# Performance work log

Measured on AMD Instinct MI355X. Metric: run time of the kernel, lower is better.

## Reference

```python
import jax, jax.numpy as jnp
import numpy as np

D = 64      # hidden_dim
H = 4       # num_attention_heads
DH = D // H # head_dim
B = 64      # graphs per batch
SCALE = np.float32(np.sqrt(DH))


def _sage(x, edge, wl, bl, wr):
    # SAGEConv: lin_l(mean_j x_j) + lin_r(x_i); mean over incoming edges (dst = edge[1])
    src, dst = edge[0], edge[1]
    n = x.shape[0]
    agg = jax.ops.segment_sum(x[src], dst, num_segments=n)
    cnt = jax.ops.segment_sum(jnp.ones((edge.shape[1],), x.dtype), dst, num_segments=n)
    mean = agg / jnp.maximum(cnt, 1.0)[:, None]
    return mean @ wl + bl + x @ wr


def _cross_attn(xq, xk, w, b):
    # w: [3, D, D] stacked (Q, K, V) projections; b: [3, D]
    Q = (xq @ w[0] + b[0]).reshape(-1, H, DH)  # [Nq, H, DH]
    K = (xk @ w[1] + b[1]).reshape(-1, H, DH)  # [Nk, H, DH]
    V = (xk @ w[2] + b[2]).reshape(-1, H, DH)
    scores = jnp.einsum('qhd,khd->hqk', Q, K) / SCALE  # [H, Nq, Nk]
    wgt = jax.nn.softmax(scores, axis=-1)
    out = jnp.einsum('hqk,khd->qhd', wgt, V)
    return out.reshape(xq.shape[0], D)


def _segment_mean(x, seg, num):
    s = jax.ops.segment_sum(x, seg, num_segments=num)
    c = jax.ops.segment_sum(jnp.ones((x.shape[0],), x.dtype), seg, num_segments=num)
    return s / jnp.maximum(c, 1.0)[:, None]


def setup_inputs() -> dict:
    key = jax.random.key(0)
    ks = jax.random.split(key, 32)
    N_MOL, N_PROT, E_MOL, E_PROT = 2048, 8192, 32768, 131072
    MOL_IN, PROT_IN = 32, 64

    def lin(k, i, o, s=None):
        s = 1.0 / np.sqrt(i) if s is None else s
        return (jax.random.normal(k, (i, o), jnp.float32) * s)

    inp = {
        'x_mol': jax.random.normal(ks[0], (N_MOL, MOL_IN), jnp.float32),
        'x_prot': jax.random.normal(ks[1], (N_PROT, PROT_IN), jnp.float32),
        'm1_wl': lin(ks[2], MOL_IN, D), 'm1_bl': jnp.zeros((D,), jnp.float32), 'm1_wr': lin(ks[3], MOL_IN, D),
        'm2_wl': lin(ks[4], D, D), 'm2_bl': jnp.zeros((D,), jnp.float32), 'm2_wr': lin(ks[5], D, D),
        'p1_wl': lin(ks[6], PROT_IN, D), 'p1_bl': jnp.zeros((D,), jnp.float32), 'p1_wr': lin(ks[7], PROT_IN, D),
        'p2_wl': lin(ks[8], D, D), 'p2_bl': jnp.zeros((D,), jnp.float32), 'p2_wr': lin(ks[9], D, D),
        'amp_w': jax.random.normal(ks[10], (3, D, D), jnp.float32) / np.sqrt(D),
        'amp_b': jnp.zeros((3, D), jnp.float32),
        'apm_w': jax.random.normal(ks[11], (3, D, D), jnp.float32) / np.sqrt(D),
        'apm_b': jnp.zeros((3, D), jnp.float32),
        'fc1_w': lin(ks[12], 2 * D, D), 'fc1_b': jnp.zeros((D,), jnp.float32),
        'fc2_w': lin(ks[13], D, 1), 'fc2_b': jnp.zeros((1,), jnp.float32),
        'edge_mol': jax.random.randint(ks[14], (2, E_MOL), 0, N_MOL, jnp.int32),
        'edge_prot': jax.random.randint(ks[15], (2, E_PROT), 0, N_PROT, jnp.int32),
        'batch_mol': jnp.sort(jax.random.randint(ks[16], (N_MOL,), 0, B, jnp.int32)),
        'batch_prot': jnp.sort(jax.random.randint(ks[17], (N_PROT,), 0, B, jnp.int32)),
    }
    return inp


def reference(x_mol, x_prot,
              m1_wl, m1_bl, m1_wr, m2_wl, m2_bl, m2_wr,
              p1_wl, p1_bl, p1_wr, p2_wl, p2_bl, p2_wr,
              amp_w, amp_b, apm_w, apm_b,
              fc1_w, fc1_b, fc2_w, fc2_b,
              edge_mol, edge_prot, batch_mol, batch_prot):
    # two SAGE conv blocks per graph, ReLU after each (HeteroConv with one edge type)
    h_mol = jax.nn.relu(_sage(x_mol, edge_mol, m1_wl, m1_bl, m1_wr))
    h_mol = jax.nn.relu(_sage(h_mol, edge_mol, m2_wl, m2_bl, m2_wr))
    h_prot = jax.nn.relu(_sage(x_prot, edge_prot, p1_wl, p1_bl, p1_wr))
    h_prot = jax.nn.relu(_sage(h_prot, edge_prot, p2_wl, p2_bl, p2_wr))
    # cross attention (mol queries prot, prot queries mol) + residual
    h_mol_c = h_mol + _cross_attn(h_mol, h_prot, amp_w, amp_b)
    h_prot_c = h_prot + _cross_attn(h_prot, h_mol, apm_w, apm_b)
    # global mean pool per graph
    z_mol = _segment_mean(h_mol_c, batch_mol, B)    # [B, D]
    z_prot = _segment_mean(h_prot_c, batch_prot, B)  # [B, D]
    z = jnp.concatenate([z_mol, z_prot], axis=1)     # [B, 2D]
    x = jax.nn.relu(z @ fc1_w + fc1_b)
    out = jax.nn.sigmoid(x @ fc2_w + fc2_b)
    return out.squeeze(-1)  # [B]
```

## Files before the change

### kernel.cpp

```cpp
#include <hip/hip_runtime.h>
#include <math.h>

#define D 64
#define NB 64

typedef __attribute__((ext_vector_type(8))) short bf16x8;
typedef __attribute__((ext_vector_type(4))) float f32x4;
typedef __attribute__((ext_vector_type(16))) float f32x16;

#define M3(a, b, c) fmaxf(fmaxf((a), (b)), (c))

__device__ __forceinline__ unsigned short f2bf(float f) {
    unsigned u = __float_as_uint(f);
    u += 0x7FFF + ((u >> 16) & 1);
    return (unsigned short)(u >> 16);
}
__device__ __forceinline__ unsigned pk_bf16(float lo, float hi) {
    unsigned r;
    asm("v_cvt_pk_bf16_f32 %0, %1, %2" : "=v"(r) : "v"(lo), "v"(hi));
    return r;
}
__device__ __forceinline__ float fexp2(float x) {
    float r;
    asm("v_exp_f32 %0, %1" : "=v"(r) : "v"(x));
    return r;
}

__global__ void k_prep2(const int* __restrict__ em, int Em,
                        const int* __restrict__ ep, int Ep,
                        int* __restrict__ degm, int* __restrict__ degp,
                        const int* __restrict__ bm, int Nm, int* __restrict__ bsM,
                        const int* __restrict__ bp, int Np, int* __restrict__ bsP) {
    int i = blockIdx.x * blockDim.x + threadIdx.x;
    if (i < Em) atomicAdd(&degm[em[Em + i]], 1);
    int j = i - Em;
    if (j >= 0 && j < Ep) atomicAdd(&degp[ep[Ep + j]], 1);
    if (i < Nm) {
        int cur = bm[i];
        int prev = (i == 0) ? -1 : bm[i - 1];
        for (int b = prev + 1; b <= cur; ++b) bsM[b] = i;
        if (i == Nm - 1)
            for (int b = cur + 1; b <= NB; ++b) bsM[b] = Nm;
    }
    int j2 = i - Nm;
    if (j2 >= 0 && j2 < Np) {
        int cur = bp[j2];
        int prev = (j2 == 0) ? -1 : bp[j2 - 1];
        for (int b = prev + 1; b <= cur; ++b) bsP[b] = j2;
        if (j2 == Np - 1)
            for (int b = cur + 1; b <= NB; ++b) bsP[b] = Np;
    }
}

__global__ __launch_bounds__(256) void k_scan2(
        const int* __restrict__ degm, int Nm, int* __restrict__ rpm, int* __restrict__ curm,
        const int* __restrict__ degp, int Np, int* __restrict__ rpp, int* __restrict__ curp) {
    __shared__ int sdeg[8192];
    __shared__ int chunk[256];
    const int* deg = blockIdx.x ? degp : degm;
    int N = blockIdx.x ? Np : Nm;
    int* rowptr = blockIdx.x ? rpp : rpm;
    int* cursor = blockIdx.x ? curp : curm;
    int t = threadIdx.x;
    for (int i = t; i < N; i += 256) sdeg[i] = deg[i];
    __syncthreads();
    int C = (N + 255) / 256;
    int start = t * C;
    int sum = 0;
    for (int i = 0; i < C; ++i)
        if (start + i < N) sum += sdeg[start + i];
    chunk[t] = sum;
    __syncthreads();
    for (int ofs = 1; ofs < 256; ofs <<= 1) {
        int v = (t >= ofs) ? chunk[t - ofs] : 0;
        __syncthreads();
        chunk[t] += v;
        __syncthreads();
    }
    int base = (t == 0) ? 0 : chunk[t - 1];
    for (int i = 0; i < C && start + i < N; ++i) {
        rowptr[start + i] = base;
        cursor[start + i] = base;
        base += sdeg[start + i];
    }
    if (t == 255) rowptr[N] = base;
}

__global__ void k_scatter2(const int* __restrict__ em, int Em, int* __restrict__ curm,
                           int* __restrict__ csrm,
                           const int* __restrict__ ep, int Ep, int* __restrict__ curp,
                           int* __restrict__ csrp) {
    int i = blockIdx.x * blockDim.x + threadIdx.x;
    if (i < Em) {
        int s = em[i], d = em[Em + i];
        csrm[atomicAdd(&curm[d], 1)] = s;
    }
    int j = i - Em;
    if (j >= 0 && j < Ep) {
        int s = ep[j], d = ep[Ep + j];
        csrp[atomicAdd(&curp[d], 1)] = s;
    }
}

template<int FIN>
__device__ __forceinline__ void gsage_body(
        const float* __restrict__ x, const int* __restrict__ rowptr,
        const int* __restrict__ csr, int N,
        const float* __restrict__ wl, const float* __restrict__ bl,
        const float* __restrict__ wr, float* __restrict__ out,
        int blk, float* __restrict__ swl, float* __restrict__ swr,
        float* __restrict__ sagg, float* __restrict__ sx) {
    for (int i = threadIdx.x; i < FIN * D; i += 256) { swl[i] = wl[i]; swr[i] = wr[i]; }
    int w = threadIdx.x >> 6;
    int lane = threadIdx.x & 63;
    int r = blk * 4 + w;
    if (r < N) {
        int e0 = rowptr[r], e1 = rowptr[r + 1];
        float inv = 1.0f / fmaxf((float)(e1 - e0), 1.0f);
        if (FIN == 64) {
            float a0 = 0.f, a1 = 0.f, a2 = 0.f, a3 = 0.f;
            int e = e0;
            for (; e + 3 < e1; e += 4) {
                a0 += x[(size_t)csr[e] * FIN + lane];
                a1 += x[(size_t)csr[e + 1] * FIN + lane];
                a2 += x[(size_t)csr[e + 2] * FIN + lane];
                a3 += x[(size_t)csr[e + 3] * FIN + lane];
            }
            for (; e < e1; ++e) a0 += x[(size_t)csr[e] * FIN + lane];
            sagg[w * 64 + lane] = ((a0 + a1) + (a2 + a3)) * inv;
            sx[w * 64 + lane] = x[(size_t)r * FIN + lane];
        } else {
            int f = lane & 31, half = lane >> 5;
            float a = 0.f;
            for (int e = e0 + half; e < e1; e += 2)
                a += x[(size_t)csr[e] * FIN + f];
            a += __shfl_xor(a, 32);
            if (half == 0) {
                sagg[w * 64 + f] = a * inv;
                sx[w * 64 + f] = x[(size_t)r * FIN + f];
            }
        }
    }
    __syncthreads();
    if (r >= N) return;
    int c = lane;
    float acc = bl[c];
    #pragma unroll 8
    for (int k = 0; k < FIN; ++k) {
        acc += sagg[w * 64 + k] * swl[k * D + c];
        acc += sx[w * 64 + k] * swr[k * D + c];
    }
    out[(size_t)r * D + c] = fmaxf(acc, 0.0f);
}

template<int FA, int FB>
__global__ __launch_bounds__(256) void k_gsage2(
        const float* __restrict__ xA, const int* __restrict__ rpA,
        const int* __restrict__ csrA, int NA,
        const float* __restrict__ wlA, const float* __restrict__ blA,
        const float* __restrict__ wrA, float* __restrict__ outA,
        const float* __restrict__ xB, const int* __restrict__ rpB,
        const int* __restrict__ csrB, int NB_,
        const float* __restrict__ wlB, const float* __restrict__ blB,
        const float* __restrict__ wrB, float* __restrict__ outB) {
    __shared__ float swl[64 * 64];
    __shared__ float swr[64 * 64];
    __shared__ float sagg[4 * 64];
    __shared__ float sx[4 * 64];
    int bA = NA / 4;
    if ((int)blockIdx.x < bA)
        gsage_body<FA>(xA, rpA, csrA, NA, wlA, blA, wrA, outA, blockIdx.x, swl, swr, sagg, sx);
    else
        gsage_body<FB>(xB, rpB, csrB, NB_, wlB, blB, wrB, outB, blockIdx.x - bA, swl, swr, sagg, sx);
}

__global__ __launch_bounds__(256) void k_qkv2(
        const float* __restrict__ xA, int NA, const float* __restrict__ xB, int NB_,
        const float* __restrict__ amp_w, const float* __restrict__ amp_b,
        const float* __restrict__ apm_w, const float* __restrict__ apm_b, float qs,
        unsigned short* __restrict__ QA, unsigned short* __restrict__ KA, unsigned short* __restrict__ VA,
        unsigned short* __restrict__ QB, unsigned short* __restrict__ KB, unsigned short* __restrict__ VB) {
    __shared__ float sq[D * D], sk[D * D], sv[D * D], sx[16 * D];
    int bA = NA / 16;
    const float *x, *wq, *bq, *wk, *bk, *wv, *bv;
    unsigned short *oq, *ok, *ov;
    int blk;
    if ((int)blockIdx.x < bA) {
        x = xA; blk = blockIdx.x;
        wq = amp_w;        bq = amp_b;
        wk = apm_w + 4096; bk = apm_b + 64;
        wv = apm_w + 8192; bv = apm_b + 128;
        oq = QA; ok = KA; ov = VA;
    } else {
        x = xB; blk = blockIdx.x - bA;
        wq = apm_w;        bq = apm_b;
        wk = amp_w + 4096; bk = amp_b + 64;
        wv = amp_w + 8192; bv = amp_b + 128;
        oq = QB; ok = KB; ov = VB;
    }
    for (int i = threadIdx.x; i < D * D; i += 256) { sq[i] = wq[i]; sk[i] = wk[i]; sv[i] = wv[i]; }
    int rbase = blk * 16;
    for (int i = threadIdx.x; i < 16 * D; i += 256) sx[i] = x[(size_t)rbase * D + i];
    __syncthreads();
    int c = threadIdx.x & 63;
    int r0 = (threadIdx.x >> 6) * 4;
    for (int rr = 0; rr < 4; ++rr) {
        int r = r0 + rr;
        float aq = bq[c], ak = bk[c], av = bv[c];
        #pragma unroll 8
        for (int k = 0; k < D; ++k) {
            float xv = sx[r * D + k];
            aq += xv * sq[k * D + c];
            ak += xv * sk[k * D + c];
            av += xv * sv[k * D + c];
        }
        size_t o = (size_t)(rbase + r) * D + c;
        oq[o] = f2bf(aq * qs);
        ok[o] = f2bf(ak);
        ov[o] = f2bf(av);
    }
}

__global__ void k_transp2(const unsigned short* __restrict__ inM, unsigned short* __restrict__ outM, int Nm,
                          const unsigned short* __restrict__ inP, unsigned short* __restrict__ outP, int Np) {
    __shared__ unsigned short tile[64][72];
    int bm = Nm >> 6;
    const unsigned short* in; unsigned short* out; int N;
    int blk = blockIdx.x;
    if (blk < bm) { in = inM; out = outM; N = Nm; }
    else { blk -= bm; in = inP; out = outP; N = Np; }
    int t = threadIdx.x;
    int rbase = blk * 64;
    {
        int r = t >> 2, c0 = (t & 3) * 16;
        const uint4* src = (const uint4*)(in + (size_t)(rbase + r) * 64 + c0);
        uint4 a = src[0], b = src[1];
        *(uint4*)(&tile[r][c0]) = a;
        *(uint4*)(&tile[r][c0 + 8]) = b;
    }
    __syncthreads();
    {
        int c = t >> 2, r0 = (t & 3) * 16;
        union { uint2 v2[4]; unsigned short s[16]; } u;
        #pragma unroll
        for (int i = 0; i < 16; ++i) u.s[i] = tile[r0 + i][c];
        int key0 = rbase + r0;
        int kc = key0 & ~31;
        int b16 = key0 & 16;
        unsigned short* op = out + (size_t)c * N;
        const int gmap[4] = {0, 8, 4, 12};
        #pragma unroll
        for (int b = 0; b < 4; ++b)
            *(uint2*)(op + kc + b16 + gmap[b]) = u.v2[b];
    }
    if (t < 8) {
        uint4 ones;
        ones.x = ones.y = ones.z = ones.w = 0x3F803F80u;
        *(uint4*)(out + (size_t)64 * N + rbase + t * 8) = ones;
    }
}

#define MAXTREE(cm, s0, s1)                                                   \
    {                                                                         \
        float c0 = M3(s0[0], s0[1], s0[2]);                                   \
        float c1 = M3(s0[3], s0[4], s0[5]);                                   \
        float c2 = M3(s0[6], s0[7], s0[8]);                                   \
        float c3 = M3(s0[9], s0[10], s0[11]);                                 \
        float c4 = M3(s0[12], s0[13], s0[14]);                                \
        float c5 = M3(s0[15], s1[0], s1[1]);                                  \
        float c6 = M3(s1[2], s1[3], s1[4]);                                   \
        float c7 = M3(s1[5], s1[6], s1[7]);                                   \
        float c8 = M3(s1[8], s1[9], s1[10]);                                  \
        float c9 = M3(s1[11], s1[12], s1[13]);                                \
        float ca = fmaxf(s1[14], s1[15]);                                     \
        float d0 = M3(c0, c1, c2);                                            \
        float d1 = M3(c3, c4, c5);                                            \
        float d2 = M3(c6, c7, c8);                                            \
        float d3 = M3(c9, ca, d0);                                            \
        cm = M3(d1, d2, d3);                                                  \
    }

#define PVPACK(S, KB)                                                         \
    {                                                                         \
        union { unsigned u[4]; bf16x8 v; } f1, f2;                            \
        f1.u[0] = pk_bf16((S)[0], (S)[1]);   f1.u[1] = pk_bf16((S)[2], (S)[3]);  \
        f1.u[2] = pk_bf16((S)[4], (S)[5]);   f1.u[3] = pk_bf16((S)[6], (S)[7]);  \
        f2.u[0] = pk_bf16((S)[8], (S)[9]);   f2.u[1] = pk_bf16((S)[10], (S)[11]);\
        f2.u[2] = pk_bf16((S)[12], (S)[13]); f2.u[3] = pk_bf16((S)[14], (S)[15]);\
        bf16x8 vb0 = *(const bf16x8*)(vbase + (KB) + half * 8);               \
        bf16x8 vb1 = *(const bf16x8*)(vbase + (KB) + 16 + half * 8);          \
        __builtin_amdgcn_s_setprio(1);                                        \
        o = __builtin_amdgcn_mfma_f32_32x32x16_bf16(f1.v, vb0, o, 0, 0, 0);   \
        o = __builtin_amdgcn_mfma_f32_32x32x16_bf16(f2.v, vb1, o, 0, 0, 0);   \
        __builtin_amdgcn_s_setprio(0);                                        \
    }

__global__ __launch_bounds__(512) void k_attn6(
        const unsigned short* __restrict__ QmB, const unsigned short* __restrict__ KpB,
        const unsigned short* __restrict__ VpT, int Nm, int Np, int lsm,
        float* __restrict__ poM, float* __restrict__ pmM, float* __restrict__ plM,
        const unsigned short* __restrict__ QpB, const unsigned short* __restrict__ KmB,
        const unsigned short* __restrict__ VmT, int lsp,
        float* __restrict__ poP, float* __restrict__ pmP, float* __restrict__ plP) {
    const unsigned short *Q, *K, *Vt;
    int Nq, Nk, ls;
    float *po, *pm, *pl;
    if (blockIdx.y == 0) { Q = QmB; K = KpB; Vt = VpT; Nq = Nm; Nk = Np; ls = lsm; po = poM; pm = pmM; pl = plM; }
    else                 { Q = QpB; K = KmB; Vt = VmT; Nq = Np; Nk = Nm; ls = lsp; po = poP; pm = pmP; pl = plP; }
    int npair = Nq >> 6;
    if ((int)blockIdx.x >= (npair << ls)) return;
    const int qpair = blockIdx.x >> ls;
    const int split = blockIdx.x & ((1 << ls) - 1);
    const int kchunk = Nk >> ls;
    const int w = threadIdx.x >> 6;
    const int h = w & 3;
    const int qt = qpair * 2 + (w >> 2);
    const int lane = threadIdx.x & 63;
    const int cq = lane & 31;
    const int half = lane >> 5;
    const int h16 = h * 16;

    bf16x8 qb = *(const bf16x8*)(Q + ((size_t)(qt * 32 + cq) * D + h16 + half * 8));
    int drow = (cq < 16) ? (h16 + cq) : (cq == 16 ? 64 : h16 + 15);
    const unsigned short* vbase = Vt + (size_t)drow * Nk;

    f32x16 o, mC;
    #pragma unroll
    for (int i = 0; i < 16; ++i) { o[i] = 0.f; mC[i] = 0.f; }
    float m;

    const int kstart = split * kchunk;
    {
        const int kb = kstart;
        bf16x8 ka0 = *(const bf16x8*)(K + ((size_t)(kb + cq) * D + h16 + half * 8));
        bf16x8 ka1 = *(const bf16x8*)(K + ((size_t)(kb + 32 + cq) * D + h16 + half * 8));
        f32x16 s0 = __builtin_amdgcn_mfma_f32_32x32x16_bf16(ka0, qb, mC, 0, 0, 0);
        f32x16 s1 = __builtin_amdgcn_mfma_f32_32x32x16_bf16(ka1, qb, mC, 0, 0, 0);
        float cm;
        MAXTREE(cm, s0, s1);
        #pragma unroll
        for (int off = 1; off < 64; off <<= 1) cm = fmaxf(cm, __shfl_xor(cm, off));
        m = cm;
        #pragma unroll
        for (int i = 0; i < 16; ++i) {
            s0[i] = fexp2(s0[i] - m);
            s1[i] = fexp2(s1[i] - m);
            mC[i] = -m;
        }
        PVPACK(s0, kb)
        PVPACK(s1, kb + 32)
    }
    for (int kb = kstart + 64; kb < kstart + kchunk; kb += 64) {
        bf16x8 ka0 = *(const bf16x8*)(K + ((size_t)(kb + cq) * D + h16 + half * 8));
        bf16x8 ka1 = *(const bf16x8*)(K + ((size_t)(kb + 32 + cq) * D + h16 + half * 8));
        f32x16 s0 = __builtin_amdgcn_mfma_f32_32x32x16_bf16(ka0, qb, mC, 0, 0, 0);
        f32x16 s1 = __builtin_amdgcn_mfma_f32_32x32x16_bf16(ka1, qb, mC, 0, 0, 0);
        float cm;
        MAXTREE(cm, s0, s1);
        if (__any(cm > 8.f)) {
            float cw = cm;
            #pragma unroll
            for (int off = 1; off < 64; off <<= 1) cw = fmaxf(cw, __shfl_xor(cw, off));
            float nm = fmaxf(m + cw, m);
            float sc = fexp2(m - nm);
            #pragma unroll
            for (int i = 0; i < 16; ++i) o[i] *= sc;
            float dl = nm - m;
            #pragma unroll
            for (int i = 0; i < 16; ++i) { s0[i] -= dl; s1[i] -= dl; mC[i] = -nm; }
            m = nm;
        }
        #pragma unroll
        for (int i = 0; i < 16; ++i) { s0[i] = fexp2(s0[i]); s1[i] = fexp2(s1[i]); }
        PVPACK(s0, kb)
        PVPACK(s1, kb + 32)
    }

    size_t pbase = (size_t)split * Nq + qt * 32;
    if (half == 0)
        pm[(pbase + cq) * 4 + h] = m;
    if (cq == 16) {
        #pragma unroll
        for (int r = 0; r < 16; ++r) {
            int qr = (r & 3) + 8 * (r >> 2) + 4 * half;
            pl[(pbase + qr) * 4 + h] = o[r];
        }
    }
    if (cq < 16) {
        #pragma unroll
        for (int r = 0; r < 16; ++r) {
            int qr = (r & 3) + 8 * (r >> 2) + 4 * half;
            po[(pbase + qr) * 64 + h16 + cq] = o[r];
        }
    }
}

template<int NS>
__device__ __forceinline__ void comb_body(
        const float* __restrict__ po, const float* __restrict__ pm,
        const float* __restrict__ pl, int Nq,
        const float* __restrict__ resid, float* __restrict__ outc, int i) {
    int q = i >> 4;
    int part = i & 15;
    int d0 = part * 4;
    int h = part >> 2;
    float pmv[NS], plv[NS];
    #pragma unroll
    for (int s = 0; s < NS; ++s) pmv[s] = pm[((size_t)s * Nq + q) * 4 + h];
    #pragma unroll
    for (int s = 0; s < NS; ++s) plv[s] = pl[((size_t)s * Nq + q) * 4 + h];
    float M = pmv[0];
    #pragma unroll
    for (int s = 1; s < NS; ++s) M = fmaxf(M, pmv[s]);
    float4 O = {0.f, 0.f, 0.f, 0.f};
    float L = 0.f;
    #pragma unroll
    for (int s = 0; s < NS; ++s) {
        float wgt = fexp2(pmv[s] - M);
        float4 pv = *(const float4*)(po + ((size_t)s * Nq + q) * 64 + d0);
        O.x += pv.x * wgt; O.y += pv.y * wgt; O.z += pv.z * wgt; O.w += pv.w * wgt;
        L += plv[s] * wgt;
    }
    float invL = 1.0f / L;
    float4 rv = *(const float4*)(resid + (size_t)q * 64 + d0);
    float4 res;
    res.x = rv.x + O.x * invL;
    res.y = rv.y + O.y * invL;
    res.z = rv.z + O.z * invL;
    res.w = rv.w + O.w * invL;
    *(float4*)(outc + (size_t)q * 64 + d0) = res;
}

template<int NSM, int NSP>
__global__ void k_comb2t(
        const float* __restrict__ poM, const float* __restrict__ pmM, const float* __restrict__ plM,
        int Nm, const float* __restrict__ residM, float* __restrict__ outM,
        const float* __restrict__ poP, const float* __restrict__ pmP, const float* __restrict__ plP,
        int Np, const float* __restrict__ residP, float* __restrict__ outP) {
    int idx = blockIdx.x * blockDim.x + threadIdx.x;
    int mtot = Nm * 16;
    if (idx < mtot)
        comb_body<NSM>(poM, pmM, plM, Nm, residM, outM, idx);
    else if (idx - mtot < Np * 16)
        comb_body<NSP>(poP, pmP, plP, Np, residP, outP, idx - mtot);
}

__global__ void k_comb2(
        const float* __restrict__ poM, const float* __restrict__ pmM, const float* __restrict__ plM,
        int nsM, int Nm, const float* __restrict__ residM, float* __restrict__ outM,
        const float* __restrict__ poP, const float* __restrict__ pmP, const float* __restrict__ plP,
        int nsP, int Np, const float* __restrict__ residP, float* __restrict__ outP) {
    int idx = blockIdx.x * blockDim.x + threadIdx.x;
    const float *po, *pm, *pl, *resid;
    float* outc;
    int ns, Nq, i;
    int mtot = Nm * 64;
    if (idx < mtot) {
        po = poM; pm = pmM; pl = plM; ns = nsM; Nq = Nm; resid = residM; outc = outM; i = idx;
    } else {
        i = idx - mtot;
        if (i >= Np * 64) return;
        po = poP; pm = pmP; pl = plP; ns = nsP; Nq = Np; resid = residP; outc = outP;
    }
    int q = i >> 6, d = i & 63, h = d >> 4;
    float M = -1e30f;
    for (int s = 0; s < ns; ++s)
        M = fmaxf(M, pm[((size_t)s * Nq + q) * 4 + h]);
    float O = 0.f, L = 0.f;
    for (int s = 0; s < ns; ++s) {
        float wgt = fexp2(pm[((size_t)s * Nq + q) * 4 + h] - M);
        O += po[((size_t)s * Nq + q) * 64 + d] * wgt;
        L += pl[((size_t)s * Nq + q) * 4 + h] * wgt;
    }
    outc[i] = resid[i] + O / L;
}

__global__ __launch_bounds__(256) void k_pool2(
        const float* __restrict__ hM, const int* __restrict__ bsM,
        const float* __restrict__ hP, const int* __restrict__ bsP,
        float* __restrict__ zsum, float* __restrict__ zcnt) {
    __shared__ float red[4][64];
    int b = blockIdx.x & 63;
    int isP = blockIdx.x >> 6;
    const float* h = isP ? hP : hM;
    const int* bs = isP ? bsP : bsM;
    int colOff = isP ? 64 : 0;
    int n0 = bs[b], n1 = bs[b + 1];
    int w = threadIdx.x >> 6, c = threadIdx.x & 63;
    float acc = 0.f;
    for (int n = n0 + w; n < n1; n += 4)
        acc += h[(size_t)n * 64 + c];
    red[w][c] = acc;
    __syncthreads();
    if (w == 0) {
        float s = (red[0][c] + red[1][c]) + (red[2][c] + red[3][c]);
        zsum[b * 128 + colOff + c] = s;
        if (c == 0) zcnt[b * 2 + isP] = (float)(n1 - n0);
    }
}

__global__ __launch_bounds__(256) void k_head2(
        const float* __restrict__ zsum, const float* __restrict__ zcnt,
        const float* __restrict__ fc1w, const float* __restrict__ fc1b,
        const float* __restrict__ fc2w, const float* __restrict__ fc2b,
        float* __restrict__ out) {
    int b = blockIdx.x * 4 + (threadIdx.x >> 6);
    int c = threadIdx.x & 63;
    float inv0 = 1.0f / fmaxf(zcnt[b * 2 + 0], 1.0f);
    float inv1 = 1.0f / fmaxf(zcnt[b * 2 + 1], 1.0f);
    float acc = fc1b[c];
    #pragma unroll 8
    for (int k = 0; k < 128; ++k) {
        float zv = zsum[b * 128 + k] * (k < 64 ? inv0 : inv1);
        acc += zv * fc1w[k * 64 + c];
    }
    float v = fmaxf(acc, 0.0f) * fc2w[c];
    #pragma unroll
    for (int off = 32; off > 0; off >>= 1) v += __shfl_xor(v, off);
    if (c == 0) out[b] = 1.0f / (1.0f + __expf(-(v + fc2b[0])));
}

extern "C" void kernel_launch(void* const* d_in, const int* in_sizes, int n_in,
                              void* d_out, int out_size, void* d_ws, size_t ws_size,
                              hipStream_t stream) {
    const float* x_mol  = (const float*)d_in[0];
    const float* x_prot = (const float*)d_in[1];
    const float* m1_wl = (const float*)d_in[2];
    const float* m1_bl = (const float*)d_in[3];
    const float* m1_wr = (const float*)d_in[4];
    const float* m2_wl = (const float*)d_in[5];
    const float* m2_bl = (const float*)d_in[6];
    const float* m2_wr = (const float*)d_in[7];
    const float* p1_wl = (const float*)d_in[8];
    const float* p1_bl = (const float*)d_in[9];
    const float* p1_wr = (const float*)d_in[10];
    const float* p2_wl = (const float*)d_in[11];
    const float* p2_bl = (const float*)d_in[12];
    const float* p2_wr = (const float*)d_in[13];
    const float* amp_w = (const float*)d_in[14];
    const float* amp_b = (const float*)d_in[15];
    const float* apm_w = (const float*)d_in[16];
    const float* apm_b = (const float*)d_in[17];
    const float* fc1_w = (const float*)d_in[18];
    const float* fc1_b = (const float*)d_in[19];
    const float* fc2_w = (const float*)d_in[20];
    const float* fc2_b = (const float*)d_in[21];
    const int* edge_mol  = (const int*)d_in[22];
    const int* edge_prot = (const int*)d_in[23];
    const int* batch_mol  = (const int*)d_in[24];
    const int* batch_prot = (const int*)d_in[25];
    float* out = (float*)d_out;

    const int N_MOL  = in_sizes[0] / 32;
    const int N_PROT = in_sizes[1] / 64;
    const int E_MOL  = in_sizes[22] / 2;
    const int E_PROT = in_sizes[23] / 2;

    char* base = (char*)d_ws;
    size_t off = 0;
    auto alloc = [&](size_t bytes) -> void* {
        void* p = base + off;
        off = (off + bytes + 255) & ~(size_t)255;
        return p;
    };
    float* h_mol1   = (float*)alloc((size_t)N_MOL * D * sizeof(float));
    float* h_mol2   = (float*)alloc((size_t)N_MOL * D * sizeof(float));
    float* h_prot1  = (float*)alloc((size_t)N_PROT * D * sizeof(float));
    float* h_prot2  = (float*)alloc((size_t)N_PROT * D * sizeof(float));
    float* h_mol_c  = (float*)alloc((size_t)N_MOL * D * sizeof(float));
    float* h_prot_c = (float*)alloc((size_t)N_PROT * D * sizeof(float));
    float* zsum     = (float*)alloc((NB * 128 + NB * 2) * sizeof(float));
    float* zcnt     = zsum + NB * 128;
    unsigned short* Qm_b = (unsigned short*)alloc((size_t)N_MOL * D * 2);
    unsigned short* Km_b = (unsigned short*)alloc((size_t)N_MOL * D * 2);
    unsigned short* Vm_b = (unsigned short*)alloc((size_t)N_MOL * D * 2);
    unsigned short* Vm_t = (unsigned short*)alloc((size_t)N_MOL * (D + 1) * 2);
    unsigned short* Qp_b = (unsigned short*)alloc((size_t)N_PROT * D * 2);
    unsigned short* Kp_b = (unsigned short*)alloc((size_t)N_PROT * D * 2);
    unsigned short* Vp_b = (unsigned short*)alloc((size_t)N_PROT * D * 2);
    unsigned short* Vp_t = (unsigned short*)alloc((size_t)N_PROT * (D + 1) * 2);
    int* deg      = (int*)alloc(((size_t)N_MOL + N_PROT) * sizeof(int));
    int* deg_m    = deg;
    int* deg_p    = deg + N_MOL;
    int* rp_m     = (int*)alloc(((size_t)N_MOL + 1) * sizeof(int));
    int* cur_m    = (int*)alloc((size_t)N_MOL * sizeof(int));
    int* csr_m    = (int*)alloc((size_t)E_MOL * sizeof(int));
    int* rp_p     = (int*)alloc(((size_t)N_PROT + 1) * sizeof(int));
    int* cur_p    = (int*)alloc((size_t)N_PROT * sizeof(int));
    int* csr_p    = (int*)alloc((size_t)E_PROT * sizeof(int));
    int* bsM      = (int*)alloc((NB + 1) * sizeof(int));
    int* bsP      = (int*)alloc((NB + 1) * sizeof(int));

    int nsm = 16; while (nsm > 1 && (N_PROT % (64 * nsm))) nsm >>= 1;
    int nsp = 4;  while (nsp > 1 && (N_MOL % (64 * nsp)))  nsp >>= 1;
    int lsm = 31 - __builtin_clz(nsm);
    int lsp = 31 - __builtin_clz(nsp);
    float* poM = (float*)alloc((size_t)nsm * N_MOL * 64 * sizeof(float));
    float* pmM = (float*)alloc((size_t)nsm * N_MOL * 4 * sizeof(float));
    float* plM = (float*)alloc((size_t)nsm * N_MOL * 4 * sizeof(float));
    float* poP = (float*)alloc((size_t)nsp * N_PROT * 64 * sizeof(float));
    float* pmP = (float*)alloc((size_t)nsp * N_PROT * 4 * sizeof(float));
    float* plP = (float*)alloc((size_t)nsp * N_PROT * 4 * sizeof(float));

    const int BLK = 256;
    dim3 blk(BLK);
    const float QS = 0.25f * 1.4426950408889634f;

    hipMemsetAsync(deg, 0, ((size_t)N_MOL + N_PROT) * sizeof(int), stream);
    int Etot = E_MOL + E_PROT;
    k_prep2<<<(Etot + BLK - 1) / BLK, blk, 0, stream>>>(
        edge_mol, E_MOL, edge_prot, E_PROT, deg_m, deg_p,
        batch_mol, N_MOL, bsM, batch_prot, N_PROT, bsP);
    k_scan2<<<2, blk, 0, stream>>>(deg_m, N_MOL, rp_m, cur_m, deg_p, N_PROT, rp_p, cur_p);
    k_scatter2<<<(Etot + BLK - 1) / BLK, blk, 0, stream>>>(edge_mol, E_MOL, cur_m, csr_m,
                                                           edge_prot, E_PROT, cur_p, csr_p);

    k_gsage2<32, 64><<<N_MOL / 4 + N_PROT / 4, blk, 0, stream>>>(
        x_mol,  rp_m, csr_m, N_MOL,  m1_wl, m1_bl, m1_wr, h_mol1,
        x_prot, rp_p, csr_p, N_PROT, p1_wl, p1_bl, p1_wr, h_prot1);
    k_gsage2<64, 64><<<N_MOL / 4 + N_PROT / 4, blk, 0, stream>>>(
        h_mol1,  rp_m, csr_m, N_MOL,  m2_wl, m2_bl, m2_wr, h_mol2,
        h_prot1, rp_p, csr_p, N_PROT, p2_wl, p2_bl, p2_wr, h_prot2);

    k_qkv2<<<N_MOL / 16 + N_PROT / 16, blk, 0, stream>>>(
        h_mol2, N_MOL, h_prot2, N_PROT, amp_w, amp_b, apm_w, apm_b, QS,
        Qm_b, Km_b, Vm_b, Qp_b, Kp_b, Vp_b);

    k_transp2<<<N_MOL / 64 + N_PROT / 64, blk, 0, stream>>>(Vm_b, Vm_t, N_MOL, Vp_b, Vp_t, N_PROT);

    int gxm = (N_MOL / 64) * nsm;
    int gxp = (N_PROT / 64) * nsp;
    int gx = gxm > gxp ? gxm : gxp;
    k_attn6<<<dim3(gx, 2), dim3(512), 0, stream>>>(
        Qm_b, Kp_b, Vp_t, N_MOL, N_PROT, lsm, poM, pmM, plM,
        Qp_b, Km_b, Vm_t, lsp, poP, pmP, plP);

    if (nsm == 16 && nsp == 4) {
        int tot = (N_MOL + N_PROT) * 16;
        k_comb2t<16, 4><<<(tot + BLK - 1) / BLK, blk, 0, stream>>>(
            poM, pmM, plM, N_MOL, h_mol2, h_mol_c,
            poP, pmP, plP, N_PROT, h_prot2, h_prot_c);
    } else {
        k_comb2<<<((N_MOL + N_PROT) * 64 + BLK - 1) / BLK, blk, 0, stream>>>(
            poM, pmM, plM, nsm, N_MOL, h_mol2, h_mol_c,
            poP, pmP, plP, nsp, N_PROT, h_prot2, h_prot_c);
    }

    k_pool2<<<128, blk, 0, stream>>>(h_mol_c, bsM, h_prot_c, bsP, zsum, zcnt);

    k_head2<<<16, blk, 0, stream>>>(zsum, zcnt, fc1_w, fc1_b, fc2_w, fc2_b, out);
}
```

Measured before the change: 171.9 us.

## Fuse V transpose into QKV, merge pool and head, batch SAGE rows

The V transpose now happens inside the QKV projection kernel: V is staged as bf16 in shared memory and written straight into the transposed, swizzled layout, including the ones row, so the separate transpose kernel and its intermediate buffer go away. Global pooling and the MLP head are merged into one kernel that runs one block per graph. The SAGE kernel now handles 16 rows per block instead of 4, so the weight load into shared memory is paid over more rows. This cuts two launches and some global traffic, but it lowers block counts and parallelism in the SAGE, QKV and pool kernels.

```diff
diff --git a/kernel.cpp b/kernel.cpp
--- a/kernel.cpp
+++ b/kernel.cpp
@@ -103,7 +103,7 @@
 }
 
 template<int FIN>
-__device__ __forceinline__ void gsage_body(
+__device__ __forceinline__ void gsage3_body(
         const float* __restrict__ x, const int* __restrict__ rowptr,
         const int* __restrict__ csr, int N,
         const float* __restrict__ wl, const float* __restrict__ bl,
@@ -111,10 +111,12 @@
         int blk, float* __restrict__ swl, float* __restrict__ swr,
         float* __restrict__ sagg, float* __restrict__ sx) {
     for (int i = threadIdx.x; i < FIN * D; i += 256) { swl[i] = wl[i]; swr[i] = wr[i]; }
+    __syncthreads();
     int w = threadIdx.x >> 6;
     int lane = threadIdx.x & 63;
-    int r = blk * 4 + w;
-    if (r < N) {
+    for (int rr = 0; rr < 4; ++rr) {
+        int r = blk * 16 + w * 4 + rr;
+        if (r >= N) return;
         int e0 = rowptr[r], e1 = rowptr[r + 1];
         float inv = 1.0f / fmaxf((float)(e1 - e0), 1.0f);
         if (FIN == 64) {
@@ -140,21 +142,19 @@
                 sx[w * 64 + f] = x[(size_t)r * FIN + f];
             }
         }
-    }
-    __syncthreads();
-    if (r >= N) return;
-    int c = lane;
-    float acc = bl[c];
-    #pragma unroll 8
-    for (int k = 0; k < FIN; ++k) {
-        acc += sagg[w * 64 + k] * swl[k * D + c];
-        acc += sx[w * 64 + k] * swr[k * D + c];
-    }
-    out[(size_t)r * D + c] = fmaxf(acc, 0.0f);
+        int c = lane;
+        float acc = bl[c];
+        #pragma unroll 8
+        for (int k = 0; k < FIN; ++k) {
+            acc += sagg[w * 64 + k] * swl[k * D + c];
+            acc += sx[w * 64 + k] * swr[k * D + c];
+        }
+        out[(size_t)r * D + c] = fmaxf(acc, 0.0f);
+    }
 }
 
 template<int FA, int FB>
-__global__ __launch_bounds__(256) void k_gsage2(
+__global__ __launch_bounds__(256) void k_gsage3(
         const float* __restrict__ xA, const int* __restrict__ rpA,
         const int* __restrict__ csrA, int NA,
         const float* __restrict__ wlA, const float* __restrict__ blA,
@@ -167,44 +167,48 @@
     __shared__ float swr[64 * 64];
     __shared__ float sagg[4 * 64];
     __shared__ float sx[4 * 64];
-    int bA = NA / 4;
+    int bA = (NA + 15) / 16;
     if ((int)blockIdx.x < bA)
-        gsage_body<FA>(xA, rpA, csrA, NA, wlA, blA, wrA, outA, blockIdx.x, swl, swr, sagg, sx);
+        gsage3_body<FA>(xA, rpA, csrA, NA, wlA, blA, wrA, outA, blockIdx.x, swl, swr, sagg, sx);
     else
-        gsage_body<FB>(xB, rpB, csrB, NB_, wlB, blB, wrB, outB, blockIdx.x - bA, swl, swr, sagg, sx);
-}
-
-__global__ __launch_bounds__(256) void k_qkv2(
+        gsage3_body<FB>(xB, rpB, csrB, NB_, wlB, blB, wrB, outB, blockIdx.x - bA, swl, swr, sagg, sx);
+}
+
+__global__ __launch_bounds__(256) void k_qkv3(
         const float* __restrict__ xA, int NA, const float* __restrict__ xB, int NB_,
         const float* __restrict__ amp_w, const float* __restrict__ amp_b,
         const float* __restrict__ apm_w, const float* __restrict__ apm_b, float qs,
-        unsigned short* __restrict__ QA, unsigned short* __restrict__ KA, unsigned short* __restrict__ VA,
-        unsigned short* __restrict__ QB, unsigned short* __restrict__ KB, unsigned short* __restrict__ VB) {
-    __shared__ float sq[D * D], sk[D * D], sv[D * D], sx[16 * D];
-    int bA = NA / 16;
+        unsigned short* __restrict__ QA, unsigned short* __restrict__ KA,
+        unsigned short* __restrict__ VtA,
+        unsigned short* __restrict__ QB, unsigned short* __restrict__ KB,
+        unsigned short* __restrict__ VtB) {
+    __shared__ float sq[D * D], sk[D * D], sv[D * D];
+    __shared__ float sx[32 * D];
+    __shared__ unsigned short svo[32][68];
+    int bA = NA / 32;
     const float *x, *wq, *bq, *wk, *bk, *wv, *bv;
-    unsigned short *oq, *ok, *ov;
-    int blk;
+    unsigned short *oq, *ok, *vt;
+    int blk, N;
     if ((int)blockIdx.x < bA) {
-        x = xA; blk = blockIdx.x;
+        x = xA; blk = blockIdx.x; N = NA;
         wq = amp_w;        bq = amp_b;
         wk = apm_w + 4096; bk = apm_b + 64;
         wv = apm_w + 8192; bv = apm_b + 128;
-        oq = QA; ok = KA; ov = VA;
+        oq = QA; ok = KA; vt = VtA;
     } else {
-        x = xB; blk = blockIdx.x - bA;
+        x = xB; blk = blockIdx.x - bA; N = NB_;
         wq = apm_w;        bq = apm_b;
         wk = amp_w + 4096; bk = amp_b + 64;
         wv = amp_w + 8192; bv = amp_b + 128;
-        oq = QB; ok = KB; ov = VB;
+        oq = QB; ok = KB; vt = VtB;
     }
     for (int i = threadIdx.x; i < D * D; i += 256) { sq[i] = wq[i]; sk[i] = wk[i]; sv[i] = wv[i]; }
-    int rbase = blk * 16;
-    for (int i = threadIdx.x; i < 16 * D; i += 256) sx[i] = x[(size_t)rbase * D + i];
+    int rbase = blk * 32;
+    for (int i = threadIdx.x; i < 32 * D; i += 256) sx[i] = x[(size_t)rbase * D + i];
     __syncthreads();
     int c = threadIdx.x & 63;
-    int r0 = (threadIdx.x >> 6) * 4;
-    for (int rr = 0; rr < 4; ++rr) {
+    int r0 = (threadIdx.x >> 6) * 8;
+    for (int rr = 0; rr < 8; ++rr) {
         int r = r0 + rr;
         float aq = bq[c], ak = bk[c], av = bv[c];
         #pragma unroll 8
@@ -217,46 +221,29 @@
         size_t o = (size_t)(rbase + r) * D + c;
         oq[o] = f2bf(aq * qs);
         ok[o] = f2bf(ak);
-        ov[o] = f2bf(av);
-    }
-}
-
-__global__ void k_transp2(const unsigned short* __restrict__ inM, unsigned short* __restrict__ outM, int Nm,
-                          const unsigned short* __restrict__ inP, unsigned short* __restrict__ outP, int Np) {
-    __shared__ unsigned short tile[64][72];
-    int bm = Nm >> 6;
-    const unsigned short* in; unsigned short* out; int N;
-    int blk = blockIdx.x;
-    if (blk < bm) { in = inM; out = outM; N = Nm; }
-    else { blk -= bm; in = inP; out = outP; N = Np; }
-    int t = threadIdx.x;
-    int rbase = blk * 64;
-    {
-        int r = t >> 2, c0 = (t & 3) * 16;
-        const uint4* src = (const uint4*)(in + (size_t)(rbase + r) * 64 + c0);
-        uint4 a = src[0], b = src[1];
-        *(uint4*)(&tile[r][c0]) = a;
-        *(uint4*)(&tile[r][c0 + 8]) = b;
-    }
-    __syncthreads();
-    {
-        int c = t >> 2, r0 = (t & 3) * 16;
-        union { uint2 v2[4]; unsigned short s[16]; } u;
-        #pragma unroll
-        for (int i = 0; i < 16; ++i) u.s[i] = tile[r0 + i][c];
-        int key0 = rbase + r0;
-        int kc = key0 & ~31;
-        int b16 = key0 & 16;
-        unsigned short* op = out + (size_t)c * N;
-        const int gmap[4] = {0, 8, 4, 12};
-        #pragma unroll
-        for (int b = 0; b < 4; ++b)
-            *(uint2*)(op + kc + b16 + gmap[b]) = u.v2[b];
-    }
-    if (t < 8) {
+        svo[r][c] = f2bf(av);
+    }
+    __syncthreads();
+    const int gmap[4] = {0, 8, 4, 12};
+    #pragma unroll
+    for (int jj = 0; jj < 2; ++jj) {
+        int j = threadIdx.x + jj * 256;
+        int ccol = j & 63;
+        int grp = j >> 6;
+        int b16 = (grp & 4) ? 16 : 0;
+        int g = grp & 3;
+        int k0 = b16 + g * 4;
+        union { uint2 v; unsigned short s[4]; } u;
+        u.s[0] = svo[k0 + 0][ccol];
+        u.s[1] = svo[k0 + 1][ccol];
+        u.s[2] = svo[k0 + 2][ccol];
+        u.s[3] = svo[k0 + 3][ccol];
+        *(uint2*)(vt + (size_t)ccol * N + rbase + b16 + gmap[g]) = u.v;
+    }
+    if (threadIdx.x < 4) {
         uint4 ones;
         ones.x = ones.y = ones.z = ones.w = 0x3F803F80u;
-        *(uint4*)(out + (size_t)64 * N + rbase + t * 8) = ones;
+        *(uint4*)(vt + (size_t)64 * N + rbase + threadIdx.x * 8) = ones;
     }
 }
 
@@ -475,49 +462,43 @@
     outc[i] = resid[i] + O / L;
 }
 
-__global__ __launch_bounds__(256) void k_pool2(
+__global__ __launch_bounds__(256) void k_poolhead(
         const float* __restrict__ hM, const int* __restrict__ bsM,
         const float* __restrict__ hP, const int* __restrict__ bsP,
-        float* __restrict__ zsum, float* __restrict__ zcnt) {
-    __shared__ float red[4][64];
-    int b = blockIdx.x & 63;
-    int isP = blockIdx.x >> 6;
-    const float* h = isP ? hP : hM;
-    const int* bs = isP ? bsP : bsM;
-    int colOff = isP ? 64 : 0;
-    int n0 = bs[b], n1 = bs[b + 1];
-    int w = threadIdx.x >> 6, c = threadIdx.x & 63;
-    float acc = 0.f;
-    for (int n = n0 + w; n < n1; n += 4)
-        acc += h[(size_t)n * 64 + c];
-    red[w][c] = acc;
-    __syncthreads();
-    if (w == 0) {
-        float s = (red[0][c] + red[1][c]) + (red[2][c] + red[3][c]);
-        zsum[b * 128 + colOff + c] = s;
-        if (c == 0) zcnt[b * 2 + isP] = (float)(n1 - n0);
-    }
-}
-
-__global__ __launch_bounds__(256) void k_head2(
-        const float* __restrict__ zsum, const float* __restrict__ zcnt,
         const float* __restrict__ fc1w, const float* __restrict__ fc1b,
         const float* __restrict__ fc2w, const float* __restrict__ fc2b,
         float* __restrict__ out) {
-    int b = blockIdx.x * 4 + (threadIdx.x >> 6);
-    int c = threadIdx.x & 63;
-    float inv0 = 1.0f / fmaxf(zcnt[b * 2 + 0], 1.0f);
-    float inv1 = 1.0f / fmaxf(zcnt[b * 2 + 1], 1.0f);
-    float acc = fc1b[c];
-    #pragma unroll 8
-    for (int k = 0; k < 128; ++k) {
-        float zv = zsum[b * 128 + k] * (k < 64 ? inv0 : inv1);
-        acc += zv * fc1w[k * 64 + c];
-    }
-    float v = fmaxf(acc, 0.0f) * fc2w[c];
-    #pragma unroll
-    for (int off = 32; off > 0; off >>= 1) v += __shfl_xor(v, off);
-    if (c == 0) out[b] = 1.0f / (1.0f + __expf(-(v + fc2b[0])));
+    __shared__ float red[4][64];
+    __shared__ float zs[128];
+    int b = blockIdx.x;
+    int w = threadIdx.x >> 6, c = threadIdx.x & 63;
+    int n0 = bsM[b], n1 = bsM[b + 1];
+    float acc = 0.f;
+    for (int n = n0 + w; n < n1; n += 4) acc += hM[(size_t)n * 64 + c];
+    red[w][c] = acc;
+    __syncthreads();
+    if (w == 0)
+        zs[c] = ((red[0][c] + red[1][c]) + (red[2][c] + red[3][c])) /
+                fmaxf((float)(n1 - n0), 1.0f);
+    __syncthreads();
+    n0 = bsP[b]; n1 = bsP[b + 1];
+    acc = 0.f;
+    for (int n = n0 + w; n < n1; n += 4) acc += hP[(size_t)n * 64 + c];
+    red[w][c] = acc;
+    __syncthreads();
+    if (w == 0)
+        zs[64 + c] = ((red[0][c] + red[1][c]) + (red[2][c] + red[3][c])) /
+                     fmaxf((float)(n1 - n0), 1.0f);
+    __syncthreads();
+    if (w == 0) {
+        float a = fc1b[c];
+        #pragma unroll 8
+        for (int k = 0; k < 128; ++k) a += zs[k] * fc1w[k * 64 + c];
+        float v = fmaxf(a, 0.0f) * fc2w[c];
+        #pragma unroll
+        for (int off = 32; off > 0; off >>= 1) v += __shfl_xor(v, off);
+        if (c == 0) out[b] = 1.0f / (1.0f + __expf(-(v + fc2b[0])));
+    }
 }
 
 extern "C" void kernel_launch(void* const* d_in, const int* in_sizes, int n_in,
@@ -569,15 +550,11 @@
     float* h_prot2  = (float*)alloc((size_t)N_PROT * D * sizeof(float));
     float* h_mol_c  = (float*)alloc((size_t)N_MOL * D * sizeof(float));
     float* h_prot_c = (float*)alloc((size_t)N_PROT * D * sizeof(float));
-    float* zsum     = (float*)alloc((NB * 128 + NB * 2) * sizeof(float));
-    float* zcnt     = zsum + NB * 128;
     unsigned short* Qm_b = (unsigned short*)alloc((size_t)N_MOL * D * 2);
     unsigned short* Km_b = (unsigned short*)alloc((size_t)N_MOL * D * 2);
-    unsigned short* Vm_b = (unsigned short*)alloc((size_t)N_MOL * D * 2);
     unsigned short* Vm_t = (unsigned short*)alloc((size_t)N_MOL * (D + 1) * 2);
     unsigned short* Qp_b = (unsigned short*)alloc((size_t)N_PROT * D * 2);
     unsigned short* Kp_b = (unsigned short*)alloc((size_t)N_PROT * D * 2);
-    unsigned short* Vp_b = (unsigned short*)alloc((size_t)N_PROT * D * 2);
     unsigned short* Vp_t = (unsigned short*)alloc((size_t)N_PROT * (D + 1) * 2);
     int* deg      = (int*)alloc(((size_t)N_MOL + N_PROT) * sizeof(int));
     int* deg_m    = deg;
@@ -615,18 +592,17 @@
     k_scatter2<<<(Etot + BLK - 1) / BLK, blk, 0, stream>>>(edge_mol, E_MOL, cur_m, csr_m,
                                                            edge_prot, E_PROT, cur_p, csr_p);
 
-    k_gsage2<32, 64><<<N_MOL / 4 + N_PROT / 4, blk, 0, stream>>>(
+    int gs = (N_MOL + 15) / 16 + (N_PROT + 15) / 16;
+    k_gsage3<32, 64><<<gs, blk, 0, stream>>>(
         x_mol,  rp_m, csr_m, N_MOL,  m1_wl, m1_bl, m1_wr, h_mol1,
         x_prot, rp_p, csr_p, N_PROT, p1_wl, p1_bl, p1_wr, h_prot1);
-    k_gsage2<64, 64><<<N_MOL / 4 + N_PROT / 4, blk, 0, stream>>>(
+    k_gsage3<64, 64><<<gs, blk, 0, stream>>>(
         h_mol1,  rp_m, csr_m, N_MOL,  m2_wl, m2_bl, m2_wr, h_mol2,
         h_prot1, rp_p, csr_p, N_PROT, p2_wl, p2_bl, p2_wr, h_prot2);
 
-    k_qkv2<<<N_MOL / 16 + N_PROT / 16, blk, 0, stream>>>(
+    k_qkv3<<<N_MOL / 32 + N_PROT / 32, blk, 0, stream>>>(
         h_mol2, N_MOL, h_prot2, N_PROT, amp_w, amp_b, apm_w, apm_b, QS,
-        Qm_b, Km_b, Vm_b, Qp_b, Kp_b, Vp_b);
-
-    k_transp2<<<N_MOL / 64 + N_PROT / 64, blk, 0, stream>>>(Vm_b, Vm_t, N_MOL, Vp_b, Vp_t, N_PROT);
+        Qm_b, Km_b, Vm_t, Qp_b, Kp_b, Vp_t);
 
     int gxm = (N_MOL / 64) * nsm;
     int gxp = (N_PROT / 64) * nsp;
@@ -646,7 +622,6 @@
             poP, pmP, plP, nsp, N_PROT, h_prot2, h_prot_c);
     }
 
-    k_pool2<<<128, blk, 0, stream>>>(h_mol_c, bsM, h_prot_c, bsP, zsum, zcnt);
-
-    k_head2<<<16, blk, 0, stream>>>(zsum, zcnt, fc1_w, fc1_b, fc2_w, fc2_b, out);
-}
+    k_poolhead<<<NB, blk, 0, stream>>>(h_mol_c, bsM, h_prot_c, bsP,
+                                       fc1_w, fc1_b, fc2_w, fc2_b, out);
+}
```

After: 173.1 us (median of 2 runs). No clear change (+0.7%).
